# Kernel tuning notes

Hardware: AMD Instinct MI355X
Metric: run time of the kernel (lower is better)

## Reference

```python
import jax, jax.numpy as jnp
import numpy as np

STRIDES = (2, 2, 2, 2)
ALPHA = 1.0
NEG_SLOPE = 0.1


def _conv1d(h, w, b, stride):
    # h: (N, C, L), w: (O, I, K) -> (N, O, L_out), VALID padding
    out = jax.lax.conv_general_dilated(
        h, w, window_strides=(stride,), padding='VALID',
        dimension_numbers=('NCH', 'OIH', 'NCH'))
    return out + b[None, :, None]


def setup_inputs() -> dict:
    key = jax.random.key(0)
    ks = jax.random.split(key, 10)
    N, C, L = 256, 128, 1024
    k_sizes = (15, 12, 7, 4)
    inp = {'x': jax.random.normal(ks[0], (N, C, L), dtype=jnp.float32)}
    for i, k in enumerate(k_sizes):
        fan_in = C * k
        scale = 1.0 / np.sqrt(fan_in).astype(np.float32)
        inp[f'w{i+1}'] = jax.random.normal(ks[1 + 2 * i], (C, C, k), dtype=jnp.float32) * scale
        inp[f'b{i+1}'] = jax.random.normal(ks[2 + 2 * i], (C,), dtype=jnp.float32) * 0.01
    D = C * 59  # flattened encoder output: 1024->505->247->121->59
    inp['centers'] = jax.random.normal(ks[9], (64, D), dtype=jnp.float32)
    return inp


def reference(x, w1, b1, w2, b2, w3, b3, w4, b4, centers):
    ws = [(w1, b1), (w2, b2), (w3, b3), (w4, b4)]
    h = x
    for i, ((w, b), s) in enumerate(zip(ws, STRIDES)):
        h = _conv1d(h, w, b, s)
        if i != len(ws) - 1:
            h = jnp.where(h > 0, h, NEG_SLOPE * h)  # LeakyReLU(0.1)
    z = h.reshape(h.shape[0], -1)  # (N, D)
    # squared distances via norm expansion: ||z||^2 + ||c||^2 - 2 z.c
    d2 = (jnp.sum(z * z, axis=1, keepdims=True)
          + jnp.sum(centers * centers, axis=1)[None, :]
          - 2.0 * z @ centers.T)  # (N, K)
    q = 1.0 / (1.0 + d2 / ALPHA)
    q = q ** ((ALPHA + 1.0) / 2.0)
    q = q / jnp.sum(q, axis=1, keepdims=True)
    return q
```

## Files before the change

kernel.cpp:

```cpp
#include <hip/hip_runtime.h>

typedef __bf16 bf16;
typedef __bf16 bf16x4 __attribute__((ext_vector_type(4)));
typedef __bf16 bf16x8 __attribute__((ext_vector_type(8)));
typedef float f32x4 __attribute__((ext_vector_type(4)));

#define CCH 128

__global__ void k_prep_wall(const float* __restrict__ w1, const float* __restrict__ w2,
                            const float* __restrict__ w3, const float* __restrict__ w4,
                            bf16* __restrict__ o1, bf16* __restrict__ o2,
                            bf16* __restrict__ o3, bf16* __restrict__ o4) {
    int idx = blockIdx.x * 256 + threadIdx.x;
    const float* src; bf16* dst; int Kw; int r = idx;
    if (r < 15 * 16384) { src = w1; dst = o1; Kw = 15; }
    else if ((r -= 15 * 16384) < 12 * 16384) { src = w2; dst = o2; Kw = 12; }
    else if ((r -= 12 * 16384) < 7 * 16384) { src = w3; dst = o3; Kw = 7; }
    else if ((r -= 7 * 16384) < 4 * 16384) { src = w4; dst = o4; Kw = 4; }
    else return;
    int e = r & 7, lane = (r >> 3) & 63, og = (r >> 9) & 7, c = (r >> 12) & 3, kt = r >> 14;
    int o = og * 16 + (lane & 15);
    int i = c * 32 + (lane >> 4) * 8 + e;
    dst[r] = (bf16)src[(o * 128 + i) * Kw + kt];
}

__global__ __launch_bounds__(256, 8) void k_prep_x(const float* __restrict__ x,
                                                   bf16* __restrict__ xT) {
    constexpr int S = 130;
    __shared__ __align__(16) bf16 lds[64 * S];
    const int n = blockIdx.y;
    const int p0 = blockIdx.x * 64;
    const int tid = threadIdx.x;
#pragma unroll
    for (int it = 0; it < 8; ++it) {
        int u = tid + it * 256;
        int ch = u >> 4;
        int v = u & 15;
        f32x4 t = *(const f32x4*)(x + ((size_t)n * CCH + ch) * 1024 + p0 + v * 4);
#pragma unroll
        for (int e = 0; e < 4; ++e) lds[(v * 4 + e) * S + ch] = (bf16)t[e];
    }
    __syncthreads();
    bf16* op = xT + ((size_t)n * 1024 + p0) * CCH;
#pragma unroll
    for (int it = 0; it < 4; ++it) {
        int u = tid + it * 256;
        int p = u >> 4;
        int g = u & 15;
        *(bf16x8*)(op + p * CCH + g * 8) = *(const bf16x8*)(lds + p * S + g * 8);
    }
}

__global__ void k_prep_c(const float* __restrict__ c, bf16* __restrict__ cbp,
                         float* __restrict__ cc) {
    int k = blockIdx.x;
    int tid = threadIdx.x;
    float s = 0.f;
    for (int idx = tid; idx < 64 * 128; idx += 256) {
        int l = idx >> 7;
        int o = idx & 127;
        float v = (l < 59) ? c[k * 7552 + o * 59 + l] : 0.f;
        bf16 b = (bf16)v;
        cbp[(size_t)k * 64 * 128 + idx] = b;
        float fv = (float)b;
        s += fv * fv;
    }
    __shared__ float red[256];
    red[tid] = s;
    __syncthreads();
    for (int st = 128; st > 0; st >>= 1) {
        if (tid < st) red[tid] += red[tid + st];
        __syncthreads();
    }
    if (tid == 0) cc[k] = red[0];
}

template <int KW, int IN_CAP, int OUT_ROWS, int LT, int PH, bool ACT>
__global__ __launch_bounds__(256, 4) void k_conv(
    const bf16* __restrict__ in_, const bf16* __restrict__ wTp,
    const float* __restrict__ bias, bf16* __restrict__ out) {
    constexpr int P = (LT - 1) * 2 + KW;
    constexpr int CPP = 128 / PH;
    constexpr int KC = CPP / 32;
    constexpr int C16N = CPP / 8;
    constexpr int RS = CPP;
    constexpr int KCL = (KC == 4) ? 2 : 1;
    constexpr int NLT = LT / 16;
    constexpr int ESE = 136;
    constexpr int SMELE = (P * RS > LT * ESE) ? P * RS : LT * ESE;
    constexpr int NJ = KW * KC;
    __shared__ __align__(16) bf16 smem[SMELE];

    const int n = blockIdx.y;
    const int l0 = blockIdx.x * LT;
    const int p0 = l0 * 2;
    const int tid = threadIdx.x;
    const int wid = tid >> 6;
    const int lane = tid & 63;
    const int quad = lane >> 4;
    const int l15 = lane & 15;
    const int og0 = wid * 2;

    f32x4 acc[2][NLT];
#pragma unroll
    for (int a = 0; a < 2; ++a)
#pragma unroll
        for (int b = 0; b < NLT; ++b) acc[a][b] = (f32x4){0.f, 0.f, 0.f, 0.f};

    bf16x8 afr[2][2];
    const bf16* wbase = wTp + (size_t)lane * 8;

    afr[0][0] = *(const bf16x8*)(wbase + ((size_t)(og0 + 0) << 9));
    afr[0][1] = *(const bf16x8*)(wbase + ((size_t)(og0 + 1) << 9));

#pragma unroll 1
    for (int ph = 0; ph < PH; ++ph) {
        if (ph) __syncthreads();

        constexpr int UNITS = P * C16N;
        constexpr int NIT = (UNITS + 255) / 256;
        const bf16* base = in_ + ((size_t)n * IN_CAP + p0) * CCH + ph * CPP;
#pragma unroll
        for (int it = 0; it < NIT; ++it) {
            int u = tid + it * 256;
            if ((UNITS & 255) == 0 || u < UNITS) {
                int p = u >> ((C16N == 16) ? 4 : 3);
                int c = u & (C16N - 1);
                bf16x8 t = *(const bf16x8*)(base + (size_t)p * CCH + c * 8);
                int sc = (PH == 2) ? (c ^ ((p >> 1) & 7))
                                   : ((c & 8) | ((c & 7) ^ ((p >> 1) & 7)));
                *(bf16x8*)(smem + p * RS + sc * 8) = t;
            }
        }
        __syncthreads();

#pragma unroll 2
        for (int j = 0; j < NJ; ++j) {
            int nj = j + 1, nph = ph;
            if (nj == NJ) { nj = 0; ++nph; }
            if (nph < PH) {
                int kt1 = nj >> KCL;
                int c1 = (nj & (KC - 1)) + nph * KC;
                const bf16* wp = wbase + ((size_t)((kt1 * 4 + c1) * 8 + og0) << 9);
                afr[(j + 1) & 1][0] = *(const bf16x8*)(wp);
                afr[(j + 1) & 1][1] = *(const bf16x8*)(wp + 512);
            }
            const int kt = j >> KCL;
            const int c16l = (j & (KC - 1)) * 4 + quad;
#pragma unroll
            for (int lt = 0; lt < NLT; ++lt) {
                int p = (lt * 16 + l15) * 2 + kt;
                int sc = (PH == 2) ? (c16l ^ ((p >> 1) & 7))
                                   : ((c16l & 8) | ((c16l & 7) ^ ((p >> 1) & 7)));
                bf16x8 bfr = *(const bf16x8*)(smem + p * RS + sc * 8);
                acc[0][lt] = __builtin_amdgcn_mfma_f32_16x16x32_bf16(
                    afr[j & 1][0], bfr, acc[0][lt], 0, 0, 0);
                acc[1][lt] = __builtin_amdgcn_mfma_f32_16x16x32_bf16(
                    afr[j & 1][1], bfr, acc[1][lt], 0, 0, 0);
            }
        }
    }

    __syncthreads();
#pragma unroll
    for (int ot = 0; ot < 2; ++ot) {
        const int o0 = wid * 32 + ot * 16 + quad * 4;
        const f32x4 bv = *(const f32x4*)(bias + o0);
#pragma unroll
        for (int lt = 0; lt < NLT; ++lt) {
            const int l = lt * 16 + l15;
            bf16x4 pk;
#pragma unroll
            for (int r = 0; r < 4; ++r) {
                float v = acc[ot][lt][r] + bv[r];
                if (ACT) v = (v > 0.f) ? v : 0.1f * v;
                pk[r] = (bf16)v;
            }
            *(bf16x4*)(smem + l * ESE + o0) = pk;
        }
    }
    __syncthreads();
    constexpr int SNIT = LT * 16 / 256;
    bf16* op = out + ((size_t)n * OUT_ROWS + l0) * CCH;
#pragma unroll
    for (int it = 0; it < SNIT; ++it) {
        int u = tid + it * 256;
        int l = u >> 4;
        int g = u & 15;
        *(bf16x8*)(op + l * CCH + g * 8) = *(const bf16x8*)(smem + l * ESE + g * 8);
    }
}

__global__ __launch_bounds__(512, 1) void k_conv4_dist(
    const bf16* __restrict__ in_, const bf16* __restrict__ wTp,
    const float* __restrict__ bias, const bf16* __restrict__ cbp,
    const float* __restrict__ cc, float* __restrict__ out) {
    constexpr int P = 130, NJ = 16;
    constexpr int ESE = 136;
    __shared__ __align__(16) bf16 smem[P * 128];
    __shared__ __align__(16) bf16 zmem[64 * ESE];
    __shared__ float d2s[64];

    const int n = blockIdx.x;
    const int tid = threadIdx.x;
    const int wid = tid >> 6;
    const int lane = tid & 63;
    const int quad = lane >> 4;
    const int l15 = lane & 15;

    f32x4 acc[4];
#pragma unroll
    for (int b = 0; b < 4; ++b) acc[b] = (f32x4){0.f, 0.f, 0.f, 0.f};

    bf16x8 afr[2];
    const bf16* wbase = wTp + (size_t)lane * 8;
    afr[0] = *(const bf16x8*)(wbase + ((size_t)wid << 9));

    {
        constexpr int UNITS = P * 16;
        const bf16* base = in_ + (size_t)n * 128 * CCH;
#pragma unroll
        for (int it = 0; it < 5; ++it) {
            int u = tid + it * 512;
            if (u < UNITS) {
                int p = u >> 4;
                int c = u & 15;
                bf16x8 t = *(const bf16x8*)(base + (size_t)p * CCH + c * 8);
                int sc = (c & 8) | ((c & 7) ^ ((p >> 1) & 7));
                *(bf16x8*)(smem + p * 128 + sc * 8) = t;
            }
        }
    }
    __syncthreads();

#pragma unroll 2
    for (int j = 0; j < NJ; ++j) {
        if (j + 1 < NJ) {
            int kt1 = (j + 1) >> 2;
            int c1 = (j + 1) & 3;
            afr[(j + 1) & 1] =
                *(const bf16x8*)(wbase + ((size_t)((kt1 * 4 + c1) * 8 + wid) << 9));
        }
        const int kt = j >> 2;
        const int c16l = (j & 3) * 4 + quad;
#pragma unroll
        for (int lt = 0; lt < 4; ++lt) {
            int p = (lt * 16 + l15) * 2 + kt;
            int sc = (c16l & 8) | ((c16l & 7) ^ ((p >> 1) & 7));
            bf16x8 bfr = *(const bf16x8*)(smem + p * 128 + sc * 8);
            acc[lt] = __builtin_amdgcn_mfma_f32_16x16x32_bf16(afr[j & 1], bfr, acc[lt], 0, 0, 0);
        }
    }

    {
        const int o0 = wid * 16 + quad * 4;
        const f32x4 bv = *(const f32x4*)(bias + o0);
#pragma unroll
        for (int lt = 0; lt < 4; ++lt) {
            const int l = lt * 16 + l15;
            bf16x4 pk;
#pragma unroll
            for (int r = 0; r < 4; ++r) {
                float v = acc[lt][r] + bv[r];
                pk[r] = (l < 59) ? (bf16)v : (bf16)0.f;
            }
            *(bf16x4*)(zmem + l * ESE + o0) = pk;
        }
    }
    __syncthreads();

#pragma unroll 1
    for (int cp = 0; cp < 8; ++cp) {
        const int kc = cp * 8 + wid;
        const bf16* cr = cbp + (size_t)kc * 8192;
        float t = 0.f;
#pragma unroll
        for (int it = 0; it < 16; ++it) {
            int ci = it * 64 + lane;
            int l = ci >> 4;
            int g = ci & 15;
            bf16x8 cv = *(const bf16x8*)(cr + ci * 8);
            bf16x8 zv = *(const bf16x8*)(zmem + l * ESE + g * 8);
#pragma unroll
            for (int e = 0; e < 8; ++e) {
                float zf = (float)zv[e];
                t += zf * (zf - 2.f * (float)cv[e]);
            }
        }
#pragma unroll
        for (int o = 32; o > 0; o >>= 1) t += __shfl_xor(t, o);
        if (lane == 0) d2s[kc] = t + cc[kc];
    }
    __syncthreads();
    if (tid < 64) {
        float q = 1.f / (1.f + d2s[tid]);
        float tot = q;
#pragma unroll
        for (int o = 32; o > 0; o >>= 1) tot += __shfl_xor(tot, o);
        out[n * 64 + tid] = q / tot;
    }
}

extern "C" void kernel_launch(void* const* d_in, const int* in_sizes, int n_in,
                              void* d_out, int out_size, void* d_ws, size_t ws_size,
                              hipStream_t stream) {
    (void)in_sizes; (void)n_in; (void)out_size; (void)ws_size;
    const float* x   = (const float*)d_in[0];
    const float* w1  = (const float*)d_in[1];
    const float* b1  = (const float*)d_in[2];
    const float* w2  = (const float*)d_in[3];
    const float* b2  = (const float*)d_in[4];
    const float* w3  = (const float*)d_in[5];
    const float* b3  = (const float*)d_in[6];
    const float* w4  = (const float*)d_in[7];
    const float* b4  = (const float*)d_in[8];
    const float* cen = (const float*)d_in[9];
    float* out = (float*)d_out;

    char* ws = (char*)d_ws;
    size_t off = 0;
    auto alloc = [&](size_t bytes) -> void* {
        void* p = ws + off;
        off += (bytes + 255) & ~(size_t)255;
        return p;
    };
    bf16* wT1 = (bf16*)alloc((size_t)15 * 16384 * sizeof(bf16));
    bf16* wT2 = (bf16*)alloc((size_t)12 * 16384 * sizeof(bf16));
    bf16* wT3 = (bf16*)alloc((size_t)7 * 16384 * sizeof(bf16));
    bf16* wT4 = (bf16*)alloc((size_t)4 * 16384 * sizeof(bf16));
    bf16* cbp = (bf16*)alloc((size_t)64 * 64 * 128 * sizeof(bf16));
    float* cc = (float*)alloc(64 * sizeof(float));
    bf16* h1  = (bf16*)alloc((size_t)256 * 512 * 128 * sizeof(bf16));
    bf16* xT  = (bf16*)alloc((size_t)256 * 1024 * 128 * sizeof(bf16));
    bf16* h2  = xT;
    bf16* h3  = h1;
    (void)alloc((size_t)1 << 20);

    k_prep_wall<<<(38 * 16384 + 255) / 256, 256, 0, stream>>>(w1, w2, w3, w4, wT1, wT2, wT3, wT4);
    k_prep_c<<<64, 256, 0, stream>>>(cen, cbp, cc);
    k_prep_x<<<dim3(16, 256), 256, 0, stream>>>(x, xT);

    k_conv<15, 1024, 512, 128, 2, true>
        <<<dim3(4, 256), 256, 0, stream>>>(xT, wT1, b1, h1);
    k_conv<12, 512, 256, 64, 1, true>
        <<<dim3(4, 256), 256, 0, stream>>>(h1, wT2, b2, h2);
    k_conv<7, 256, 128, 32, 1, true>
        <<<dim3(4, 256), 256, 0, stream>>>(h2, wT3, b3, h3);
    k_conv4_dist<<<256, 512, 0, stream>>>(h3, wT4, b4, cbp, cc, out);
}
```

Before: 374.3 us.

## Fuse fp32-to-bf16 input transpose into first conv kernel

Removes the separate k_prep_x pass that converted x to a channels-last bf16 buffer. The new k_conv1 reads fp32 x directly, converts it and transposes it into swizzled LDS tiles per channel phase, then runs the same MFMA loop with bias and LeakyReLU. This avoids writing and re-reading a 64MB intermediate and one kernel launch. In exchange, conv1 does strided fp32 loads with scalar LDS stores and reloads overlapping halo columns for each tile.

Result: faster. 342.4 us (-8.5%).

```diff
diff --git a/kernel.cpp b/kernel.cpp
--- a/kernel.cpp
+++ b/kernel.cpp
@@ -24,33 +24,6 @@
     dst[r] = (bf16)src[(o * 128 + i) * Kw + kt];
 }
 
-__global__ __launch_bounds__(256, 8) void k_prep_x(const float* __restrict__ x,
-                                                   bf16* __restrict__ xT) {
-    constexpr int S = 130;
-    __shared__ __align__(16) bf16 lds[64 * S];
-    const int n = blockIdx.y;
-    const int p0 = blockIdx.x * 64;
-    const int tid = threadIdx.x;
-#pragma unroll
-    for (int it = 0; it < 8; ++it) {
-        int u = tid + it * 256;
-        int ch = u >> 4;
-        int v = u & 15;
-        f32x4 t = *(const f32x4*)(x + ((size_t)n * CCH + ch) * 1024 + p0 + v * 4);
-#pragma unroll
-        for (int e = 0; e < 4; ++e) lds[(v * 4 + e) * S + ch] = (bf16)t[e];
-    }
-    __syncthreads();
-    bf16* op = xT + ((size_t)n * 1024 + p0) * CCH;
-#pragma unroll
-    for (int it = 0; it < 4; ++it) {
-        int u = tid + it * 256;
-        int p = u >> 4;
-        int g = u & 15;
-        *(bf16x8*)(op + p * CCH + g * 8) = *(const bf16x8*)(lds + p * S + g * 8);
-    }
-}
-
 __global__ void k_prep_c(const float* __restrict__ c, bf16* __restrict__ cbp,
                          float* __restrict__ cc) {
     int k = blockIdx.x;
@@ -73,6 +46,125 @@
         __syncthreads();
     }
     if (tid == 0) cc[k] = red[0];
+}
+
+__global__ __launch_bounds__(256, 4) void k_conv1(
+    const float* __restrict__ x, const bf16* __restrict__ wTp,
+    const float* __restrict__ bias, bf16* __restrict__ out) {
+    constexpr int KW = 15, LT = 128, PH = 2, OUT_ROWS = 512;
+    constexpr int P = (LT - 1) * 2 + KW;
+    constexpr int CPP = 64;
+    constexpr int KC = 2;
+    constexpr int RS = CPP;
+    constexpr int NLT = LT / 16;
+    constexpr int ESE = 136;
+    constexpr int SMELE = (P * RS > LT * ESE) ? P * RS : LT * ESE;
+    constexpr int NJ = KW * KC;
+    __shared__ __align__(16) bf16 smem[SMELE];
+
+    const int n = blockIdx.y;
+    const int l0 = blockIdx.x * LT;
+    const int p0 = l0 * 2;
+    const int tid = threadIdx.x;
+    const int wid = tid >> 6;
+    const int lane = tid & 63;
+    const int quad = lane >> 4;
+    const int l15 = lane & 15;
+    const int og0 = wid * 2;
+
+    f32x4 acc[2][NLT];
+#pragma unroll
+    for (int a = 0; a < 2; ++a)
+#pragma unroll
+        for (int b = 0; b < NLT; ++b) acc[a][b] = (f32x4){0.f, 0.f, 0.f, 0.f};
+
+    bf16x8 afr[2][2];
+    const bf16* wbase = wTp + (size_t)lane * 8;
+    afr[0][0] = *(const bf16x8*)(wbase + ((size_t)(og0 + 0) << 9));
+    afr[0][1] = *(const bf16x8*)(wbase + ((size_t)(og0 + 1) << 9));
+
+    const int cst = tid >> 2;
+    const int qw = tid & 3;
+
+#pragma unroll 1
+    for (int ph = 0; ph < PH; ++ph) {
+        if (ph) __syncthreads();
+
+        const float* bch = x + ((size_t)(n * 128 + ph * 64 + cst)) * 1024;
+#pragma unroll 4
+        for (int it = 0; it < 17; ++it) {
+            int pp = it * 16 + qw * 4;
+            int gp = p0 + pp;
+            f32x4 t;
+            if (gp + 3 < 1024) {
+                t = *(const f32x4*)(bch + gp);
+            } else {
+#pragma unroll
+                for (int e = 0; e < 4; ++e) t[e] = (gp + e < 1024) ? bch[gp + e] : 0.f;
+            }
+#pragma unroll
+            for (int e = 0; e < 4; ++e) {
+                int ppe = pp + e;
+                int sc8 = (((cst >> 3) ^ ((ppe >> 1) & 7)) << 3) | (cst & 7);
+                smem[ppe * RS + sc8] = (bf16)t[e];
+            }
+        }
+        __syncthreads();
+
+#pragma unroll 2
+        for (int j = 0; j < NJ; ++j) {
+            int nj = j + 1, nph = ph;
+            if (nj == NJ) { nj = 0; ++nph; }
+            if (nph < PH) {
+                int kt1 = nj >> 1;
+                int c1 = (nj & (KC - 1)) + nph * KC;
+                const bf16* wp = wbase + ((size_t)((kt1 * 4 + c1) * 8 + og0) << 9);
+                afr[(j + 1) & 1][0] = *(const bf16x8*)(wp);
+                afr[(j + 1) & 1][1] = *(const bf16x8*)(wp + 512);
+            }
+            const int kt = j >> 1;
+            const int c16l = (j & (KC - 1)) * 4 + quad;
+#pragma unroll
+            for (int lt = 0; lt < NLT; ++lt) {
+                int p = (lt * 16 + l15) * 2 + kt;
+                int sc = c16l ^ ((p >> 1) & 7);
+                bf16x8 bfr = *(const bf16x8*)(smem + p * RS + sc * 8);
+                acc[0][lt] = __builtin_amdgcn_mfma_f32_16x16x32_bf16(
+                    afr[j & 1][0], bfr, acc[0][lt], 0, 0, 0);
+                acc[1][lt] = __builtin_amdgcn_mfma_f32_16x16x32_bf16(
+                    afr[j & 1][1], bfr, acc[1][lt], 0, 0, 0);
+            }
+        }
+    }
+
+    __syncthreads();
+#pragma unroll
+    for (int ot = 0; ot < 2; ++ot) {
+        const int o0 = wid * 32 + ot * 16 + quad * 4;
+        const f32x4 bv = *(const f32x4*)(bias + o0);
+#pragma unroll
+        for (int lt = 0; lt < NLT; ++lt) {
+            const int l = lt * 16 + l15;
+            bf16x4 pk;
+#pragma unroll
+            for (int r = 0; r < 4; ++r) {
+                float v = acc[ot][lt][r] + bv[r];
+                v = (v > 0.f) ? v : 0.1f * v;
+                pk[r] = (bf16)v;
+            }
+            *(bf16x4*)(smem + l * ESE + o0) = pk;
+        }
+    }
+    __syncthreads();
+    constexpr int SNIT = LT * 16 / 256;
+    bf16* op = out + ((size_t)n * OUT_ROWS + l0) * CCH;
+#pragma unroll
+    for (int it = 0; it < SNIT; ++it) {
+        int u = tid + it * 256;
+        int l = u >> 4;
+        int g = u & 15;
+        *(bf16x8*)(op + l * CCH + g * 8) = *(const bf16x8*)(smem + l * ESE + g * 8);
+    }
 }
 
 template <int KW, int IN_CAP, int OUT_ROWS, int LT, int PH, bool ACT>
@@ -331,17 +423,14 @@
     bf16* cbp = (bf16*)alloc((size_t)64 * 64 * 128 * sizeof(bf16));
     float* cc = (float*)alloc(64 * sizeof(float));
     bf16* h1  = (bf16*)alloc((size_t)256 * 512 * 128 * sizeof(bf16));
-    bf16* xT  = (bf16*)alloc((size_t)256 * 1024 * 128 * sizeof(bf16));
-    bf16* h2  = xT;
+    bf16* h2  = (bf16*)alloc((size_t)256 * 256 * 128 * sizeof(bf16));
     bf16* h3  = h1;
     (void)alloc((size_t)1 << 20);
 
     k_prep_wall<<<(38 * 16384 + 255) / 256, 256, 0, stream>>>(w1, w2, w3, w4, wT1, wT2, wT3, wT4);
     k_prep_c<<<64, 256, 0, stream>>>(cen, cbp, cc);
-    k_prep_x<<<dim3(16, 256), 256, 0, stream>>>(x, xT);
-
-    k_conv<15, 1024, 512, 128, 2, true>
-        <<<dim3(4, 256), 256, 0, stream>>>(xT, wT1, b1, h1);
+
+    k_conv1<<<dim3(4, 256), 256, 0, stream>>>(x, wT1, b1, h1);
     k_conv<12, 512, 256, 64, 1, true>
         <<<dim3(4, 256), 256, 0, stream>>>(h1, wT2, b2, h2);
     k_conv<7, 256, 128, 32, 1, true>
```
